# Kernel optimization log

Hardware: AMD Instinct MI355X
Metric: run time of the kernel (lower is better)

The kernel has to match this reference:

```python
import jax, jax.numpy as jnp
import numpy as np
import math

L = 32            # one_side_length; seq_len = L*L = 1024
EMBED = 768
NDIM = 16
N_SSM = 768
DIRS = 4
K = DIRS * N_SSM  # kernel_dim = 3072
REPEAT = EMBED // N_SSM
SCALE = math.sqrt(1.0 / NDIM)


def _compute_kernel(A_angle, A_radius, B1p, B2p, C1p, C2p):
    # Polar-parameterized complex diagonal A's (4 transition coeffs), sigmoid B, raw C.
    ang = jax.nn.sigmoid(A_angle) * (2.0 * math.pi)
    rad = jax.nn.sigmoid(A_radius)
    A = (rad * jnp.cos(ang) + 1j * (rad * jnp.sin(ang))).astype(jnp.complex64)  # (4,K,NDIM)
    A1, A2, A3, A4 = A[0], A[1], A[2], A[3]
    sB1 = jax.nn.sigmoid(B1p); sB2 = jax.nn.sigmoid(B2p)
    B1 = (sB1[..., 0] + 1j * sB1[..., 1]).astype(jnp.complex64)   # (K,NDIM)
    B2 = (sB2[..., 0] + 1j * sB2[..., 1]).astype(jnp.complex64)
    C1 = (C1p[..., 0] + 1j * C1p[..., 1]).astype(jnp.complex64)
    C2 = (C2p[..., 0] + 1j * C2p[..., 1]).astype(jnp.complex64)

    zeros = jnp.zeros((L, K, NDIM), jnp.complex64)

    # 2-D SSM impulse response (same math the torch module precomputes via the
    # vandermonde / coefficient-table expansion):
    #   x_h[i,j] = A1 x_h[i,j-1] + A2 x_v[i,j-1] + B1 delta[i,j]
    #   x_v[i,j] = A3 x_h[i-1,j] + A4 x_v[i-1,j] + B2 delta[i,j]
    #   k[i,j]   = scale * Re(C1 . x_h[i,j] + C2 . x_v[i,j])
    def row_step(carry, i):
        xh_prev, xv_prev = carry                    # row i-1 states, (L,K,NDIM)
        first = (i == 0).astype(jnp.float32)
        xv = A3 * xh_prev + A4 * xv_prev            # vertical flow from row above
        xv = xv.at[0].add(first * B2)               # impulse at (0,0)
        h0 = (first * B1).astype(jnp.complex64)     # x_h[i,0]
        def col_step(h, v_left):
            h_new = A1 * h + A2 * v_left            # horizontal flow within the row
            return h_new, h_new
        _, xh_rest = jax.lax.scan(col_step, h0, xv[:-1])
        xh = jnp.concatenate([h0[None], xh_rest], axis=0)
        return (xh, xv), (xh, xv)

    (_, _), (XH, XV) = jax.lax.scan(row_step, (zeros, zeros), jnp.arange(L))
    # XH, XV: (L, L, K, NDIM) complex
    k = SCALE * (jnp.einsum('ijhn,hn->ijh', XH, C1) + jnp.einsum('ijhn,hn->ijh', XV, C2))
    # boundary corrections exactly as in the torch module
    k = k.at[0, :, :].multiply(2.0)
    k = k.at[:, 0, :].multiply(2.0)
    k = k.at[0, 0, :].divide(4.0)
    return k.real                                   # (L, L, K) float32


def _forward(x, A_angle, A_radius, B1p, B2p, C1p, C2p, omega):
    S, B, D = x.shape
    residual = x * omega
    k = _compute_kernel(A_angle, A_radius, B1p, B2p, C1p, C2p)
    k = jnp.transpose(k, (2, 0, 1))                 # (K, L, L)
    x4 = jnp.transpose(x, (1, 2, 0)).reshape(B, D, L, L)
    s2 = (2 * L, 2 * L)
    flips = [(), (-2,), (-1,), (-2, -1)]
    out = jnp.zeros((B, D, L, L), jnp.float32)
    for idx, fl in enumerate(flips):                # 4 scan directions via flips
        kk = jnp.tile(k[idx * N_SSM:(idx + 1) * N_SSM], (REPEAT, 1, 1))  # (D,L,L)
        xc = jnp.flip(x4, axis=fl) if fl else x4
        kf = jnp.fft.rfft2(kk, s=s2)
        xf = jnp.fft.rfft2(xc, s=s2)
        cur = jnp.fft.irfft2(xf * kf, s=s2)[..., :L, :L]
        out = out + (jnp.flip(cur, axis=fl) if fl else cur)
    out = jnp.transpose(out.reshape(B, D, S), (2, 0, 1))  # back to (S,B,D)
    return jax.nn.silu(out + residual)


def setup_inputs() -> dict:
    key = jax.random.key(0)
    ks = jax.random.split(key, 9)
    x = jax.random.normal(ks[0], (L * L, 16, EMBED), jnp.float32)
    A_angle = jax.random.uniform(ks[1], (4, K, NDIM), jnp.float32, 0.5, 3.0)
    A_radius = jax.random.uniform(ks[2], (4, K, NDIM), jnp.float32, 0.5, 3.0)
    B1p = 0.2 * jax.random.normal(ks[3], (K, NDIM, 2), jnp.float32)
    B2p = 0.2 * jax.random.normal(ks[4], (K, NDIM, 2), jnp.float32)
    C1p = jax.random.normal(ks[5], (K, NDIM, 2), jnp.float32)
    C2p = jax.random.normal(ks[6], (K, NDIM, 2), jnp.float32)
    omega = jax.random.normal(ks[7], (EMBED,), jnp.float32)
    return {"x": x, "A_angle": A_angle, "A_radius": A_radius, "B1p": B1p,
            "B2p": B2p, "C1p": C1p, "C2p": C2p, "omega": omega}


def reference(x, A_angle, A_radius, B1p, B2p, C1p, C2p, omega):
    return _forward(x, A_angle, A_radius, B1p, B2p, C1p, C2p, omega)
```

## Files before the change

kernel.cpp:

```cpp
#include <hip/hip_runtime.h>
#include <cmath>

#define TWO_PI 6.283185307179586476925f

__device__ __forceinline__ float sigm(float v) { return 1.0f / (1.0f + expf(-v)); }
__device__ __forceinline__ float2 cadd(float2 a, float2 b) { return make_float2(a.x + b.x, a.y + b.y); }
__device__ __forceinline__ float2 csub(float2 a, float2 b) { return make_float2(a.x - b.x, a.y - b.y); }
__device__ __forceinline__ float2 cmulf(float2 a, float2 b) {
    return make_float2(a.x * b.x - a.y * b.y, a.x * b.y + a.y * b.x);
}

__device__ __forceinline__ int swz(int r, int c) {
    return (r << 6) | (c ^ ((r ^ (r << 3)) & 63));
}

__device__ __forceinline__ int gfidx(int o, int m, int c) {
    return o + (c << 3) + (m << 9);
}

template<bool INV, bool HALF, bool PRUNE>
__device__ __forceinline__ void dft8(float2* x) {
    const float RS = 0.70710678118654752440f;
    float2 t0, t1, t2, t3, t4, t5, t6, t7;
    if (HALF) {
        t0 = x[0]; t4 = x[0]; t1 = x[1]; t5 = x[1];
        t2 = x[2]; t6 = x[2]; t3 = x[3]; t7 = x[3];
    } else {
        t0 = cadd(x[0], x[4]); t4 = csub(x[0], x[4]);
        t1 = cadd(x[1], x[5]); t5 = csub(x[1], x[5]);
        t2 = cadd(x[2], x[6]); t6 = csub(x[2], x[6]);
        t3 = cadd(x[3], x[7]); t7 = csub(x[3], x[7]);
    }
    float2 t5w, t6w, t7w;
    if (!INV) {
        t5w = make_float2(RS * (t5.x + t5.y), RS * (t5.y - t5.x));
        t6w = make_float2(t6.y, -t6.x);
        t7w = make_float2(RS * (t7.y - t7.x), -RS * (t7.x + t7.y));
    } else {
        t5w = make_float2(RS * (t5.x - t5.y), RS * (t5.y + t5.x));
        t6w = make_float2(-t6.y, t6.x);
        t7w = make_float2(-RS * (t7.x + t7.y), RS * (t7.x - t7.y));
    }
    float2 u0 = cadd(t0, t2), u2 = csub(t0, t2), u1 = cadd(t1, t3), dd = csub(t1, t3);
    float2 u3 = INV ? make_float2(-dd.y, dd.x) : make_float2(dd.y, -dd.x);
    x[0] = cadd(u0, u1); x[2] = cadd(u2, u3);
    if (!PRUNE) { x[4] = csub(u0, u1); x[6] = csub(u2, u3); }
    float2 v0 = cadd(t4, t6w), v2 = csub(t4, t6w), v1 = cadd(t5w, t7w), ee = csub(t5w, t7w);
    float2 v3 = INV ? make_float2(-ee.y, ee.x) : make_float2(ee.y, -ee.x);
    x[1] = cadd(v0, v1); x[3] = cadd(v2, v3);
    if (!PRUNE) { x[5] = csub(v0, v1); x[7] = csub(v2, v3); }
}

__device__ __forceinline__ void make_tw(int o, float2* tw) {
    float s, co;
    sincosf(-TWO_PI * (float)o / 64.f, &s, &co);
    tw[0] = make_float2(co, s);
#pragma unroll
    for (int k = 1; k < 7; ++k) tw[k] = cmulf(tw[k - 1], tw[0]);
}

template<bool INV, bool COL, bool HALF, bool PRUNE>
__device__ __forceinline__ void fft64(float2* a, float2* r, const float2* tw,
                                      int o, int line) {
    dft8<INV, HALF, false>(r);
#pragma unroll
    for (int k = 1; k < 8; ++k) {
        float2 w = tw[k - 1];
        if (INV) w.y = -w.y;
        r[k] = cmulf(r[k], w);
    }
#pragma unroll
    for (int m = 0; m < 8; ++m) {
        int s = 8 * o + m;
        a[COL ? swz(s, line) : swz(line, s)] = r[m];
    }
#pragma unroll
    for (int j = 0; j < 8; ++j) {
        int s = 8 * j + o;
        r[j] = a[COL ? swz(s, line) : swz(line, s)];
    }
    dft8<INV, false, PRUNE>(r);
}

__global__ __launch_bounds__(512) void ssm_gf(
        const float* __restrict__ Aang, const float* __restrict__ Arad,
        const float* __restrict__ B1p, const float* __restrict__ B2p,
        const float* __restrict__ C1p, const float* __restrict__ C2p,
        float2* __restrict__ Gf) {
    __shared__ float2 a[4096];
    int d = blockIdx.x;
    int tid = threadIdx.x;
    int w = tid >> 6;
    int t = w & 3;
    int nh = w >> 2;
    int lane = tid & 63;
    int jg = lane & 7;
    int n8 = lane >> 3;
    int n = n8 + 8 * nh;
    int c = t * 768 + d;
    int gid = c * 16 + n;

    for (int e = tid; e < 4096; e += 512) a[e] = make_float2(0.f, 0.f);

    float ar[4], ai[4];
#pragma unroll
    for (int q = 0; q < 4; ++q) {
        float ang = sigm(Aang[q * 49152 + gid]) * TWO_PI;
        float rad = sigm(Arad[q * 49152 + gid]);
        float s, co;
        sincosf(ang, &s, &co);
        ar[q] = rad * co; ai[q] = rad * s;
    }
    float a1r = ar[0], a1i = ai[0], a2r = ar[1], a2i = ai[1];
    float a3r = ar[2], a3i = ai[2], a4r = ar[3], a4i = ai[3];
    float p2r = a1r * a1r - a1i * a1i, p2i = 2.f * a1r * a1i;
    float p4r = p2r * p2r - p2i * p2i, p4i = 2.f * p2r * p2i;
    float pw3r = a1r * p2r - a1i * p2i, pw3i = a1r * p2i + a1i * p2r;

    const float2* B1v = (const float2*)B1p;
    const float2* B2v = (const float2*)B2p;
    const float2* C1v = (const float2*)C1p;
    const float2* C2v = (const float2*)C2p;
    float2 b1 = B1v[gid], b2 = B2v[gid], c1 = C1v[gid], c2 = C2v[gid];
    float b1r = sigm(b1.x), b1i = sigm(b1.y);
    float b2r = sigm(b2.x), b2i = sigm(b2.y);
    float c1r = c1.x, c1i = c1.y, c2r = c2.x, c2i = c2.y;

    __syncthreads();

    float xvr[4], xvi[4], xhr[4], xhi[4];
#pragma unroll
    for (int m = 0; m < 4; ++m) { xvr[m] = 0.f; xvi[m] = 0.f; xhr[m] = 0.f; xhi[m] = 0.f; }

    for (int i = 0; i < 32; ++i) {
#pragma unroll
        for (int m = 0; m < 4; ++m) {
            float nr = a3r * xhr[m] - a3i * xhi[m] + a4r * xvr[m] - a4i * xvi[m];
            float ni = a3r * xhi[m] + a3i * xhr[m] + a4r * xvi[m] + a4i * xvr[m];
            xvr[m] = nr; xvi[m] = ni;
        }
        if (i == 0 && jg == 0) { xvr[0] += b2r; xvi[0] += b2i; }

        float g1r = a2r * xvr[0] - a2i * xvi[0];
        float g1i = a2r * xvi[0] + a2i * xvr[0];
        float g2r = a1r * g1r - a1i * g1i + a2r * xvr[1] - a2i * xvi[1];
        float g2i = a1r * g1i + a1i * g1r + a2r * xvi[1] + a2i * xvr[1];
        float g3r = a1r * g2r - a1i * g2i + a2r * xvr[2] - a2i * xvi[2];
        float g3i = a1r * g2i + a1i * g2r + a2r * xvi[2] + a2i * xvr[2];
        float ldr = a1r * g3r - a1i * g3i + a2r * xvr[3] - a2i * xvi[3];
        float ldi = a1r * g3i + a1i * g3r + a2r * xvi[3] + a2i * xvr[3];

        float Pr = p4r, Pi = p4i, Vr = ldr, Vi = ldi;
#pragma unroll
        for (int os = 1; os <= 4; os <<= 1) {
            int src = (jg >= os) ? (lane - os) : lane;
            float Pr2 = __shfl(Pr, src, 64);
            float Pi2 = __shfl(Pi, src, 64);
            float Vr2 = __shfl(Vr, src, 64);
            float Vi2 = __shfl(Vi, src, 64);
            if (jg >= os) {
                float nPr = Pr * Pr2 - Pi * Pi2;
                float nPi = Pr * Pi2 + Pi * Pr2;
                float nVr = Pr * Vr2 - Pi * Vi2 + Vr;
                float nVi = Pr * Vi2 + Pi * Vr2 + Vi;
                Pr = nPr; Pi = nPi; Vr = nVr; Vi = nVi;
            }
        }
        int srcp = (jg >= 1) ? (lane - 1) : lane;
        float Ppr = __shfl(Pr, srcp, 64);
        float Ppi = __shfl(Pi, srcp, 64);
        float Vpr = __shfl(Vr, srcp, 64);
        float Vpi = __shfl(Vi, srcp, 64);
        float er, ei;
        if (jg == 0) {
            er = (i == 0) ? b1r : 0.f; ei = (i == 0) ? b1i : 0.f;
        } else if (i == 0) {
            er = Ppr * b1r - Ppi * b1i + Vpr;
            ei = Ppr * b1i + Ppi * b1r + Vpi;
        } else {
            er = Vpr; ei = Vpi;
        }
        xhr[0] = er; xhi[0] = ei;
        xhr[1] = a1r * er - a1i * ei + g1r;  xhi[1] = a1r * ei + a1i * er + g1i;
        xhr[2] = p2r * er - p2i * ei + g2r;  xhi[2] = p2r * ei + p2i * er + g2i;
        xhr[3] = pw3r * er - pw3i * ei + g3r; xhi[3] = pw3r * ei + pw3i * er + g3i;

        float v0 = c1r * xhr[0] - c1i * xhi[0] + c2r * xvr[0] - c2i * xvi[0];
        float v1 = c1r * xhr[1] - c1i * xhi[1] + c2r * xvr[1] - c2i * xvi[1];
        float v2 = c1r * xhr[2] - c1i * xhi[2] + c2r * xvr[2] - c2i * xvi[2];
        float v3 = c1r * xhr[3] - c1i * xhi[3] + c2r * xvr[3] - c2i * xvi[3];

        int bb0 = n8 & 1, bb1 = (n8 >> 1) & 1;
        float s0 = bb0 ? v0 : v2;
        float s1 = bb0 ? v1 : v3;
        float r0 = __shfl_xor(s0, 8, 64);
        float r1 = __shfl_xor(s1, 8, 64);
        float q0 = (bb0 ? v2 : v0) + r0;
        float q1 = (bb0 ? v3 : v1) + r1;
        float s2 = bb1 ? q0 : q1;
        float r2 = __shfl_xor(s2, 16, 64);
        float qq = (bb1 ? q1 : q0) + r2;
        qq += __shfl_xor(qq, 32, 64);
        if (n8 < 4) {
            int idx = 2 * bb0 + bb1;
            int col = 4 * jg + idx;
            float f = 0.25f;
            if (i == 0) f *= 2.f;
            if (col == 0) f *= 2.f;
            if (i == 0 && col == 0) f *= 0.25f;
            float val = f * qq;
            int rr_ = (t & 1) ? ((64 - i) & 63) : i;
            int cc_ = (t & 2) ? ((64 - col) & 63) : col;
            float* dst = ((float*)&a[swz(rr_, cc_)]) + nh;
            if (i == 0 || col == 0) atomicAdd(dst, val);
            else *dst = val;
        }
    }
    __syncthreads();
    for (int e = tid; e < 4096; e += 512) {
        float2 cv = a[e];
        a[e] = make_float2(cv.x + cv.y, 0.f);
    }
    __syncthreads();
    int o = tid & 7;
    float2 tw[7];
    make_tw(o, tw);
    {
        int row = tid >> 3;
        float2 r[8];
#pragma unroll
        for (int j = 0; j < 8; ++j) r[j] = a[swz(row, 8 * j + o)];
        fft64<false, false, false, false>(a, r, tw, o, row);
#pragma unroll
        for (int m = 0; m < 8; ++m) a[swz(row, o + 8 * m)] = r[m];
    }
    __syncthreads();
    {
        int cc = tid >> 3;
        float2 r[8];
#pragma unroll
        for (int j = 0; j < 8; ++j) r[j] = a[swz(8 * j + o, cc)];
        fft64<false, true, false, false>(a, r, tw, o, cc);
#pragma unroll
        for (int m = 0; m < 8; ++m) Gf[d * 4096 + gfidx(o, m, cc)] = r[m];
    }
}

__global__ __launch_bounds__(256) void transpose_in(const float* __restrict__ x,
                                                    float* __restrict__ xT) {
    __shared__ float t[64][65];
    int bR = blockIdx.x % 192, bS = blockIdx.x / 192;
    int r0 = bR * 64, s0 = bS * 64;
    int c = threadIdx.x & 63, w = threadIdx.x >> 6;
#pragma unroll
    for (int k = 0; k < 16; ++k) {
        int row = w + 4 * k;
        t[row][c] = x[(size_t)(s0 + row) * 12288 + r0 + c];
    }
    __syncthreads();
#pragma unroll
    for (int k = 0; k < 16; ++k) {
        int row = w + 4 * k;
        xT[(size_t)(r0 + row) * 1024 + s0 + c] = t[c][row];
    }
}

__global__ __launch_bounds__(256) void transpose_out(const float* __restrict__ xT,
                                                     float* __restrict__ out) {
    __shared__ float t[64][65];
    int bR = blockIdx.x % 192, bS = blockIdx.x / 192;
    int r0 = bR * 64, s0 = bS * 64;
    int c = threadIdx.x & 63, w = threadIdx.x >> 6;
#pragma unroll
    for (int k = 0; k < 16; ++k) {
        int row = w + 4 * k;
        t[row][c] = xT[(size_t)(r0 + row) * 1024 + s0 + c];
    }
    __syncthreads();
#pragma unroll
    for (int k = 0; k < 16; ++k) {
        int row = w + 4 * k;
        out[(size_t)(s0 + row) * 12288 + r0 + c] = t[c][row];
    }
}

__global__ __launch_bounds__(256) void conv_fft(
        const float* __restrict__ x, float* __restrict__ xT,
        const float2* __restrict__ Gf, const float* __restrict__ omega,
        float* __restrict__ out, int useT) {
    __shared__ float2 a[4096];
    int bid = (blockIdx.x & 7) * 768 + (blockIdx.x >> 3);
    int d = bid >> 3, b = (bid & 7) * 2;
    int tid = threadIdx.x;
    int o = tid & 7;
    float2 tw[7];
    make_tw(o, tw);
    const size_t base0 = (size_t)(b * 768 + d) * 1024;
    const size_t base1 = (size_t)((b + 1) * 768 + d) * 1024;
    {
        int row = tid >> 3;
        float2 r[8];
#pragma unroll
        for (int j = 0; j < 4; ++j) {
            int s2 = row * 32 + 8 * j + o;
            if (useT) r[j] = make_float2(xT[base0 + s2], xT[base1 + s2]);
            else      r[j] = make_float2(x[s2 * 12288 + b * 768 + d],
                                         x[s2 * 12288 + (b + 1) * 768 + d]);
        }
#pragma unroll
        for (int j = 4; j < 8; ++j) r[j] = make_float2(0.f, 0.f);
        fft64<false, false, true, false>(a, r, tw, o, row);
#pragma unroll
        for (int m = 0; m < 8; ++m) a[swz(row, o + 8 * m)] = r[m];
    }
    __syncthreads();
#pragma unroll 1
    for (int sw = 0; sw < 2; ++sw) {
        int c = sw * 32 + (tid >> 3);
        float2 r[8];
#pragma unroll
        for (int j = 0; j < 4; ++j) r[j] = a[swz(8 * j + o, c)];
#pragma unroll
        for (int j = 4; j < 8; ++j) r[j] = make_float2(0.f, 0.f);
        fft64<false, true, true, false>(a, r, tw, o, c);
#pragma unroll
        for (int m = 0; m < 8; ++m) {
            r[m] = cmulf(r[m], Gf[d * 4096 + gfidx(o, m, c)]);
        }
        fft64<true, true, false, true>(a, r, tw, o, c);
#pragma unroll
        for (int m = 0; m < 4; ++m) a[swz(o + 8 * m, c)] = r[m];
    }
    __syncthreads();
    {
        int row = tid >> 3;
        float2 r[8];
#pragma unroll
        for (int j = 0; j < 8; ++j) r[j] = a[swz(row, 8 * j + o)];
        fft64<true, false, false, true>(a, r, tw, o, row);
        float w = omega[d];
        const float inv = 1.0f / 4096.0f;
#pragma unroll
        for (int m = 0; m < 4; ++m) {
            int cc = o + 8 * m;
            int s2 = row * 32 + cc;
            float xa, xb;
            if (useT) { xa = xT[base0 + s2]; xb = xT[base1 + s2]; }
            else {
                xa = x[s2 * 12288 + b * 768 + d];
                xb = x[s2 * 12288 + (b + 1) * 768 + d];
            }
            float ya = r[m].x * inv + xa * w;
            float yb = r[m].y * inv + xb * w;
            float oa = ya / (1.0f + expf(-ya));
            float ob = yb / (1.0f + expf(-yb));
            if (useT) {
                xT[base0 + s2] = oa;
                xT[base1 + s2] = ob;
            } else {
                out[s2 * 12288 + b * 768 + d] = oa;
                out[s2 * 12288 + (b + 1) * 768 + d] = ob;
            }
        }
    }
}

extern "C" void kernel_launch(void* const* d_in, const int* in_sizes, int n_in,
                              void* d_out, int out_size, void* d_ws, size_t ws_size,
                              hipStream_t stream) {
    const float* x     = (const float*)d_in[0];
    const float* Aang  = (const float*)d_in[1];
    const float* Arad  = (const float*)d_in[2];
    const float* B1p   = (const float*)d_in[3];
    const float* B2p   = (const float*)d_in[4];
    const float* C1p   = (const float*)d_in[5];
    const float* C2p   = (const float*)d_in[6];
    const float* omega = (const float*)d_in[7];
    float* out = (float*)d_out;
    char* ws = (char*)d_ws;

    float2* Gf = (float2*)ws;
    float*  xT = (float*)(ws + 25165824);
    int useT = (ws_size >= (size_t)75497472) ? 1 : 0;

    ssm_gf<<<768, 512, 0, stream>>>(Aang, Arad, B1p, B2p, C1p, C2p, Gf);
    if (useT) transpose_in<<<3072, 256, 0, stream>>>(x, xT);
    conv_fft<<<6144, 256, 0, stream>>>(x, xT, Gf, omega, out, useT);
    if (useT) transpose_out<<<3072, 256, 0, stream>>>(xT, out);
}
```

Baseline: 176.8 us.

## Use DPP scan and separate boundary buffers instead of shuffles and LDS atomics

Replaces the per-row shuffle-based complex prefix scan with a DPP row-shift scan that uses precomputed power coefficients. It also swaps the xor-8 and xor-16 shuffles for DPP rotate and ds_swizzle. Row-0 and column-0 contributions now go to small side buffers, and the later real-packing pass reduces them and applies the boundary scale factors, which removes the LDS atomics. The first row is peeled out of the loop, which costs extra shared memory and some more work in the packing pass.

```diff
diff --git a/kernel.cpp b/kernel.cpp
--- a/kernel.cpp
+++ b/kernel.cpp
@@ -8,6 +8,20 @@
 __device__ __forceinline__ float2 csub(float2 a, float2 b) { return make_float2(a.x - b.x, a.y - b.y); }
 __device__ __forceinline__ float2 cmulf(float2 a, float2 b) {
     return make_float2(a.x * b.x - a.y * b.y, a.x * b.y + a.y * b.x);
+}
+
+template<int CTRL>
+__device__ __forceinline__ float dpp0(float v) {
+    return __int_as_float(__builtin_amdgcn_update_dpp(
+        0, __float_as_int(v), CTRL, 0xf, 0xf, true));
+}
+#define DPP_SHR1 0x111
+#define DPP_SHR2 0x112
+#define DPP_SHR4 0x114
+#define DPP_ROR8 0x128
+
+__device__ __forceinline__ float swz_xor16(float v) {
+    return __int_as_float(__builtin_amdgcn_ds_swizzle(__float_as_int(v), 0x401F));
 }
 
 __device__ __forceinline__ int swz(int r, int c) {
@@ -88,6 +102,8 @@
         const float* __restrict__ C1p, const float* __restrict__ C2p,
         float2* __restrict__ Gf) {
     __shared__ float2 a[4096];
+    __shared__ float row0buf[4][2][64];
+    __shared__ float col0buf[2][2][64];
     int d = blockIdx.x;
     int tid = threadIdx.x;
     int w = tid >> 6;
@@ -97,10 +113,12 @@
     int jg = lane & 7;
     int n8 = lane >> 3;
     int n = n8 + 8 * nh;
-    int c = t * 768 + d;
-    int gid = c * 16 + n;
+    int ch = t * 768 + d;
+    int gid = ch * 16 + n;
 
     for (int e = tid; e < 4096; e += 512) a[e] = make_float2(0.f, 0.f);
+    (&row0buf[0][0][0])[tid] = 0.f;
+    if (tid < 256) (&col0buf[0][0][0])[tid] = 0.f;
 
     float ar[4], ai[4];
 #pragma unroll
@@ -114,8 +132,13 @@
     float a1r = ar[0], a1i = ai[0], a2r = ar[1], a2i = ai[1];
     float a3r = ar[2], a3i = ai[2], a4r = ar[3], a4i = ai[3];
     float p2r = a1r * a1r - a1i * a1i, p2i = 2.f * a1r * a1i;
+    float p3r = a1r * p2r - a1i * p2i, p3i = a1r * p2i + a1i * p2r;
     float p4r = p2r * p2r - p2i * p2i, p4i = 2.f * p2r * p2i;
-    float pw3r = a1r * p2r - a1i * p2i, pw3i = a1r * p2i + a1i * p2r;
+    float p8r = p4r * p4r - p4i * p4i, p8i = 2.f * p4r * p4i;
+    float p16r = p8r * p8r - p8i * p8i, p16i = 2.f * p8r * p8i;
+    float cz1r = (jg >= 1) ? p4r : 0.f,  cz1i = (jg >= 1) ? p4i : 0.f;
+    float cz2r = (jg >= 2) ? p8r : 0.f,  cz2i = (jg >= 2) ? p8i : 0.f;
+    float cz4r = (jg >= 4) ? p16r : 0.f, cz4i = (jg >= 4) ? p16i : 0.f;
 
     const float2* B1v = (const float2*)B1p;
     const float2* B2v = (const float2*)B2p;
@@ -126,21 +149,30 @@
     float b2r = sigm(b2.x), b2i = sigm(b2.y);
     float c1r = c1.x, c1i = c1.y, c2r = c2.x, c2i = c2.y;
 
+    float pwr = 1.f, pwi = 0.f;
+    if (jg & 1) { pwr = p4r; pwi = p4i; }
+    if (jg & 2) { float tr = pwr * p8r - pwi * p8i;  pwi = pwr * p8i + pwi * p8r;  pwr = tr; }
+    if (jg & 4) { float tr = pwr * p16r - pwi * p16i; pwi = pwr * p16i + pwi * p16r; pwr = tr; }
+    float ebr = pwr * b1r - pwi * b1i, ebi = pwr * b1i + pwi * b1r;
+
+    int bb0 = n8 & 1, bb1 = (n8 >> 1) & 1;
+    int col = 4 * jg + 2 * bb0 + bb1;
+    int ccl = (t & 2) ? ((64 - col) & 63) : col;
+
     __syncthreads();
 
     float xvr[4], xvi[4], xhr[4], xhi[4];
 #pragma unroll
     for (int m = 0; m < 4; ++m) { xvr[m] = 0.f; xvi[m] = 0.f; xhr[m] = 0.f; xhi[m] = 0.f; }
 
-    for (int i = 0; i < 32; ++i) {
+    auto body = [&](int i, bool is0) {
 #pragma unroll
         for (int m = 0; m < 4; ++m) {
             float nr = a3r * xhr[m] - a3i * xhi[m] + a4r * xvr[m] - a4i * xvi[m];
             float ni = a3r * xhi[m] + a3i * xhr[m] + a4r * xvi[m] + a4i * xvr[m];
             xvr[m] = nr; xvi[m] = ni;
         }
-        if (i == 0 && jg == 0) { xvr[0] += b2r; xvi[0] += b2i; }
-
+        if (is0 && jg == 0) { xvr[0] += b2r; xvi[0] += b2i; }
         float g1r = a2r * xvr[0] - a2i * xvi[0];
         float g1i = a2r * xvi[0] + a2i * xvr[0];
         float g2r = a1r * g1r - a1i * g1i + a2r * xvr[1] - a2i * xvi[1];
@@ -149,77 +181,64 @@
         float g3i = a1r * g2i + a1i * g2r + a2r * xvi[2] + a2i * xvr[2];
         float ldr = a1r * g3r - a1i * g3i + a2r * xvr[3] - a2i * xvi[3];
         float ldi = a1r * g3i + a1i * g3r + a2r * xvi[3] + a2i * xvr[3];
-
-        float Pr = p4r, Pi = p4i, Vr = ldr, Vi = ldi;
-#pragma unroll
-        for (int os = 1; os <= 4; os <<= 1) {
-            int src = (jg >= os) ? (lane - os) : lane;
-            float Pr2 = __shfl(Pr, src, 64);
-            float Pi2 = __shfl(Pi, src, 64);
-            float Vr2 = __shfl(Vr, src, 64);
-            float Vi2 = __shfl(Vi, src, 64);
-            if (jg >= os) {
-                float nPr = Pr * Pr2 - Pi * Pi2;
-                float nPi = Pr * Pi2 + Pi * Pr2;
-                float nVr = Pr * Vr2 - Pi * Vi2 + Vr;
-                float nVi = Pr * Vi2 + Pi * Vr2 + Vi;
-                Pr = nPr; Pi = nPi; Vr = nVr; Vi = nVi;
-            }
-        }
-        int srcp = (jg >= 1) ? (lane - 1) : lane;
-        float Ppr = __shfl(Pr, srcp, 64);
-        float Ppi = __shfl(Pi, srcp, 64);
-        float Vpr = __shfl(Vr, srcp, 64);
-        float Vpi = __shfl(Vi, srcp, 64);
-        float er, ei;
-        if (jg == 0) {
-            er = (i == 0) ? b1r : 0.f; ei = (i == 0) ? b1i : 0.f;
-        } else if (i == 0) {
-            er = Ppr * b1r - Ppi * b1i + Vpr;
-            ei = Ppr * b1i + Ppi * b1r + Vpi;
-        } else {
-            er = Vpr; ei = Vpi;
-        }
-        xhr[0] = er; xhi[0] = ei;
-        xhr[1] = a1r * er - a1i * ei + g1r;  xhi[1] = a1r * ei + a1i * er + g1i;
-        xhr[2] = p2r * er - p2i * ei + g2r;  xhi[2] = p2r * ei + p2i * er + g2i;
-        xhr[3] = pw3r * er - pw3i * ei + g3r; xhi[3] = pw3r * ei + pw3i * er + g3i;
-
+        float Vr = ldr, Vi = ldi, sr, si;
+        sr = dpp0<DPP_SHR1>(Vr); si = dpp0<DPP_SHR1>(Vi);
+        Vr += cz1r * sr - cz1i * si; Vi += cz1r * si + cz1i * sr;
+        sr = dpp0<DPP_SHR2>(Vr); si = dpp0<DPP_SHR2>(Vi);
+        Vr += cz2r * sr - cz2i * si; Vi += cz2r * si + cz2i * sr;
+        sr = dpp0<DPP_SHR4>(Vr); si = dpp0<DPP_SHR4>(Vi);
+        Vr += cz4r * sr - cz4i * si; Vi += cz4r * si + cz4i * sr;
+        float Er = dpp0<DPP_SHR1>(Vr), Ei = dpp0<DPP_SHR1>(Vi);
+        Er = (jg == 0) ? 0.f : Er; Ei = (jg == 0) ? 0.f : Ei;
+        if (is0) { Er += ebr; Ei += ebi; }
+        xhr[0] = Er; xhi[0] = Ei;
+        xhr[1] = a1r * Er - a1i * Ei + g1r;  xhi[1] = a1r * Ei + a1i * Er + g1i;
+        xhr[2] = p2r * Er - p2i * Ei + g2r;  xhi[2] = p2r * Ei + p2i * Er + g2i;
+        xhr[3] = p3r * Er - p3i * Ei + g3r;  xhi[3] = p3r * Ei + p3i * Er + g3i;
         float v0 = c1r * xhr[0] - c1i * xhi[0] + c2r * xvr[0] - c2i * xvi[0];
         float v1 = c1r * xhr[1] - c1i * xhi[1] + c2r * xvr[1] - c2i * xvi[1];
         float v2 = c1r * xhr[2] - c1i * xhi[2] + c2r * xvr[2] - c2i * xvi[2];
         float v3 = c1r * xhr[3] - c1i * xhi[3] + c2r * xvr[3] - c2i * xvi[3];
-
-        int bb0 = n8 & 1, bb1 = (n8 >> 1) & 1;
-        float s0 = bb0 ? v0 : v2;
-        float s1 = bb0 ? v1 : v3;
-        float r0 = __shfl_xor(s0, 8, 64);
-        float r1 = __shfl_xor(s1, 8, 64);
+        float s0 = bb0 ? v0 : v2, s1 = bb0 ? v1 : v3;
+        float r0 = dpp0<DPP_ROR8>(s0), r1 = dpp0<DPP_ROR8>(s1);
         float q0 = (bb0 ? v2 : v0) + r0;
         float q1 = (bb0 ? v3 : v1) + r1;
         float s2 = bb1 ? q0 : q1;
-        float r2 = __shfl_xor(s2, 16, 64);
+        float r2 = swz_xor16(s2);
         float qq = (bb1 ? q1 : q0) + r2;
         qq += __shfl_xor(qq, 32, 64);
         if (n8 < 4) {
-            int idx = 2 * bb0 + bb1;
-            int col = 4 * jg + idx;
-            float f = 0.25f;
-            if (i == 0) f *= 2.f;
-            if (col == 0) f *= 2.f;
-            if (i == 0 && col == 0) f *= 0.25f;
-            float val = f * qq;
-            int rr_ = (t & 1) ? ((64 - i) & 63) : i;
-            int cc_ = (t & 2) ? ((64 - col) & 63) : col;
-            float* dst = ((float*)&a[swz(rr_, cc_)]) + nh;
-            if (i == 0 || col == 0) atomicAdd(dst, val);
-            else *dst = val;
-        }
-    }
+            if (is0) {
+                row0buf[t][nh][ccl] = qq;
+            } else if (col == 0) {
+                col0buf[t >> 1][nh][(t & 1) ? (64 - i) : i] = qq;
+            } else {
+                int rr_ = (t & 1) ? (64 - i) : i;
+                ((float*)&a[swz(rr_, ccl)])[nh] = qq;
+            }
+        }
+    };
+    body(0, true);
+#pragma unroll 1
+    for (int i = 1; i < 32; ++i) body(i, false);
+
     __syncthreads();
     for (int e = tid; e < 4096; e += 512) {
+        int r = e >> 6, cm = e & 63;
+        int c = cm ^ ((r ^ (r << 3)) & 63);
         float2 cv = a[e];
-        a[e] = make_float2(cv.x + cv.y, 0.f);
+        float v = cv.x + cv.y;
+        if (r == 0) {
+            v += row0buf[0][0][c] + row0buf[0][1][c] + row0buf[1][0][c] + row0buf[1][1][c]
+               + row0buf[2][0][c] + row0buf[2][1][c] + row0buf[3][0][c] + row0buf[3][1][c];
+        } else if (c == 0) {
+            v += col0buf[0][0][r] + col0buf[0][1][r] + col0buf[1][0][r] + col0buf[1][1][r];
+        }
+        float f = 0.25f;
+        if (r == 0) f *= 2.f;
+        if (c == 0) f *= 2.f;
+        if (r == 0 && c == 0) f *= 0.25f;
+        a[e] = make_float2(f * v, 0.f);
     }
     __syncthreads();
     int o = tid & 7;
```

Measured after the change: 168.3 us. 1.05x faster.
